# Performance work log

Measured on AMD Instinct MI355X. Metric: run time of the kernel, lower is better.

## Reference

```python
import jax, jax.numpy as jnp
import numpy as np
from jax import lax

DEPTH = 8
D_MODEL = 768
D_INNER = 2 * D_MODEL      # 1536
D_STATE = 16
DT_RANK = 48               # ceil(768/16)
D_CONV = 4
PATCH = 64
IN_CH = 3
IMG_H, IMG_W = 1280, 960
GRID = ((IMG_H - PATCH) // PATCH + 1, (IMG_W - PATCH) // PATCH + 1)  # (20,15)
NUM_PATCHES = GRID[0] * GRID[1]  # 300
MID = NUM_PATCHES // 2           # middle cls-token position
L = NUM_PATCHES + 1              # 301
EPS = 1e-5


def rmsnorm(x, w):
    return x * lax.rsqrt(jnp.mean(x * x, axis=-1, keepdims=True) + EPS) * w


def dwconv_causal(u, w, b):
    # u: (B,L,C), w: (C,k) depthwise, b: (C,) -- causal conv along L
    C = u.shape[-1]
    k = w.shape[-1]
    up = jnp.pad(u, ((0, 0), (k - 1, 0), (0, 0)))
    out = lax.conv_general_dilated(
        up.transpose(0, 2, 1), w[:, None, :], (1,), 'VALID',
        dimension_numbers=('NCH', 'OIH', 'NCH'), feature_group_count=C)
    return out.transpose(0, 2, 1) + b


def ssm_branch(u, convw, convb, Wx, Wdt, bdt, Alog, Dskip):
    # u: (B,L,d_inner) -> selective state-space scan output (B,L,d_inner)
    uc = jax.nn.silu(dwconv_causal(u, convw, convb))
    x_dbl = jnp.einsum('bld,ed->ble', uc, Wx)              # (B,L,dr+2*ds)
    dt, Bm, Cm = jnp.split(x_dbl, [DT_RANK, DT_RANK + D_STATE], axis=-1)
    delta = jax.nn.softplus(jnp.einsum('blr,dr->bld', dt, Wdt) + bdt)  # (B,L,di)
    A = -jnp.exp(Alog)                                     # (di, ds)

    def step(h, inp):
        d_t, B_t, C_t, u_t = inp                           # (B,di),(B,ds),(B,ds),(B,di)
        dA = jnp.exp(d_t[:, :, None] * A)                  # (B,di,ds)
        dBu = d_t[:, :, None] * B_t[:, None, :] * u_t[:, :, None]
        h = dA * h + dBu
        y = jnp.einsum('bds,bs->bd', h, C_t)
        return h, y

    Bsz = u.shape[0]
    h0 = jnp.zeros((Bsz, D_INNER, D_STATE), dtype=u.dtype)
    seq = (delta.transpose(1, 0, 2), Bm.transpose(1, 0, 2),
           Cm.transpose(1, 0, 2), uc.transpose(1, 0, 2))
    _, ys = lax.scan(step, h0, seq)
    return ys.transpose(1, 0, 2) + uc * Dskip


def _forward(x, patch_w, patch_b, cls_token, pos_embed, norm_ws,
             Win, convw_f, convb_f, Wx_f, Wdt_f, bdt_f, Alog_f, Dskip_f,
             convw_b, convb_b, Wx_b, Wdt_b, bdt_b, Alog_b, Dskip_b,
             Wout, normf_w):
    B = x.shape[0]
    # patch embed: Conv2d(3->768, k=64, s=64)
    feat = lax.conv_general_dilated(
        x, patch_w, (PATCH, PATCH), 'VALID',
        dimension_numbers=('NCHW', 'OIHW', 'NCHW')) + patch_b[None, :, None, None]
    tok = feat.reshape(B, D_MODEL, NUM_PATCHES).transpose(0, 2, 1)  # (B,300,768)
    cls = jnp.broadcast_to(cls_token, (B, 1, D_MODEL))
    tokens = jnp.concatenate([tok[:, :MID], cls, tok[:, MID:]], axis=1) + pos_embed

    def layer_step(carry, p):
        (nw, W_in, cwf, cbf, Wxf, Wdtf, bdtf, Alf, Df,
         cwb, cbb, Wxb, Wdtb, bdtb, Alb, Db, W_out) = p
        hidden, residual = carry
        residual = residual + hidden
        h = rmsnorm(residual, nw)
        xz = jnp.einsum('bld,ed->ble', h, W_in)            # (B,L,2*di)
        xs, z = jnp.split(xz, 2, axis=-1)
        yf = ssm_branch(xs, cwf, cbf, Wxf, Wdtf, bdtf, Alf, Df)
        yb = ssm_branch(xs[:, ::-1], cwb, cbb, Wxb, Wdtb, bdtb, Alb, Db)[:, ::-1]
        y = (yf + yb) * jax.nn.silu(z)
        out = jnp.einsum('ble,de->bld', y, W_out) / 2.0    # if_divide_out=True
        return (out, residual), None

    params = (norm_ws, Win, convw_f, convb_f, Wx_f, Wdt_f, bdt_f, Alog_f, Dskip_f,
              convw_b, convb_b, Wx_b, Wdt_b, bdt_b, Alog_b, Dskip_b, Wout)
    (hidden, residual), _ = lax.scan(
        layer_step, (tokens, jnp.zeros_like(tokens)), params)
    return rmsnorm(residual + hidden, normf_w)


def setup_inputs() -> dict:
    key = jax.random.key(0)
    ks = jax.random.split(key, 24)
    B = 2
    s = 0.02
    inv_sp = float(np.log(np.expm1(0.01)))  # softplus^-1(0.01)
    inp = {
        'x': jax.random.normal(ks[0], (B, IN_CH, IMG_H, IMG_W), jnp.float32),
        'patch_w': jax.random.normal(ks[1], (D_MODEL, IN_CH, PATCH, PATCH), jnp.float32) * s,
        'patch_b': jnp.zeros((D_MODEL,), jnp.float32),
        'cls_token': jax.random.normal(ks[2], (1, 1, D_MODEL), jnp.float32) * s,
        'pos_embed': jax.random.normal(ks[3], (1, L, D_MODEL), jnp.float32) * s,
        'norm_ws': jnp.ones((DEPTH, D_MODEL), jnp.float32),
        'Win': jax.random.normal(ks[4], (DEPTH, 2 * D_INNER, D_MODEL), jnp.float32) * s,
        'convw_f': jax.random.normal(ks[5], (DEPTH, D_INNER, D_CONV), jnp.float32) * 0.2,
        'convb_f': jnp.zeros((DEPTH, D_INNER), jnp.float32),
        'Wx_f': jax.random.normal(ks[6], (DEPTH, DT_RANK + 2 * D_STATE, D_INNER), jnp.float32) * s,
        'Wdt_f': jax.random.normal(ks[7], (DEPTH, D_INNER, DT_RANK), jnp.float32) * 0.1,
        'bdt_f': jnp.full((DEPTH, D_INNER), inv_sp, jnp.float32),
        'Alog_f': jnp.broadcast_to(jnp.log(jnp.arange(1, D_STATE + 1, dtype=jnp.float32)), (DEPTH, D_INNER, D_STATE)).copy(),
        'Dskip_f': jnp.ones((DEPTH, D_INNER), jnp.float32),
        'convw_b': jax.random.normal(ks[8], (DEPTH, D_INNER, D_CONV), jnp.float32) * 0.2,
        'convb_b': jnp.zeros((DEPTH, D_INNER), jnp.float32),
        'Wx_b': jax.random.normal(ks[9], (DEPTH, DT_RANK + 2 * D_STATE, D_INNER), jnp.float32) * s,
        'Wdt_b': jax.random.normal(ks[10], (DEPTH, D_INNER, DT_RANK), jnp.float32) * 0.1,
        'bdt_b': jnp.full((DEPTH, D_INNER), inv_sp, jnp.float32),
        'Alog_b': jnp.broadcast_to(jnp.log(jnp.arange(1, D_STATE + 1, dtype=jnp.float32)), (DEPTH, D_INNER, D_STATE)).copy(),
        'Dskip_b': jnp.ones((DEPTH, D_INNER), jnp.float32),
        'Wout': jax.random.normal(ks[11], (DEPTH, D_MODEL, D_INNER), jnp.float32) * s,
        'normf_w': jnp.ones((D_MODEL,), jnp.float32),
    }
    return inp


def reference(x, patch_w, patch_b, cls_token, pos_embed, norm_ws,
              Win, convw_f, convb_f, Wx_f, Wdt_f, bdt_f, Alog_f, Dskip_f,
              convw_b, convb_b, Wx_b, Wdt_b, bdt_b, Alog_b, Dskip_b,
              Wout, normf_w):
    return _forward(x, patch_w, patch_b, cls_token, pos_embed, norm_ws,
                    Win, convw_f, convb_f, Wx_f, Wdt_f, bdt_f, Alog_f, Dskip_f,
                    convw_b, convb_b, Wx_b, Wdt_b, bdt_b, Alog_b, Dskip_b,
                    Wout, normf_w)
```

## Files before the change

kernel.cpp:

```cpp
#include <hip/hip_runtime.h>
#include <hip/hip_bf16.h>
#include <math.h>

typedef unsigned short ushort_t;
typedef __attribute__((ext_vector_type(8))) short bf16x8;
typedef __attribute__((ext_vector_type(4))) float f32x4;

#define B_    2
#define L_    301
#define MID_  150
#define DM_   768
#define DI_   1536
#define DS_   16
#define DR_   48
#define XD_   80
#define NP_   300
#define EPS_  1e-5f
#define TP_   40

__device__ __forceinline__ float bf2f(ushort_t u) {
  union { float f; unsigned int i; } v; v.i = ((unsigned int)u) << 16; return v.f;
}
__device__ __forceinline__ ushort_t f2bf(float f) {
  __hip_bfloat16 h = __float2bfloat16(f);
  return *reinterpret_cast<ushort_t*>(&h);
}
__device__ __forceinline__ float silu_f(float x) { return x / (1.f + __expf(-x)); }
__device__ __forceinline__ float softplus_f(float x) {
  return fmaxf(x, 0.f) + log1pf(__expf(-fabsf(x)));
}

__device__ __forceinline__ float ld1(const void* p, size_t i, int bf) {
  if (bf) return bf2f(((const ushort_t*)p)[i]);
  return ((const float*)p)[i];
}
__device__ __forceinline__ float4 ld4(const void* p, size_t i, int bf) {
  if (bf) {
    uint2 r = *(const uint2*)((const ushort_t*)p + i);
    return make_float4(bf2f((ushort_t)(r.x & 0xffffu)), bf2f((ushort_t)(r.x >> 16)),
                       bf2f((ushort_t)(r.y & 0xffffu)), bf2f((ushort_t)(r.y >> 16)));
  }
  return *(const float4*)((const float*)p + i);
}

__device__ __forceinline__ float quad_sum(float x) {
  int a = __builtin_amdgcn_mov_dpp(__float_as_int(x), 0xB1, 0xF, 0xF, true);
  float s = x + __int_as_float(a);
  int b = __builtin_amdgcn_mov_dpp(__float_as_int(s), 0x4E, 0xF, 0xF, true);
  return s + __int_as_float(b);
}

__global__ void detect_dtype(const unsigned int* __restrict__ w, int* __restrict__ flag) {
  *flag = (w[0] == 0x3F803F80u) ? 1 : 0;
}

__global__ __launch_bounds__(256) void gemm64(
    const void* A0, const void* A1, int abf, int lda,
    const void* W0, const void* W1, size_t Woff,
    void* C0, void* C1, int cbf, int ldc,
    const void* bias0, const void* bias1, size_t boff,
    int M, int N, int K, int kc_len, int nbr,
    int mode, float scale,
    const ushort_t* gyf0, const ushort_t* gyb0, const ushort_t* gz,
    const void* nwp, size_t nwoff,
    const int* __restrict__ dflag)
{
  const int bf = *dflag;
  const int br = blockIdx.z % nbr;
  const int kc = blockIdx.z / nbr;
  const void* A = br ? A1 : A0;
  const void* W = br ? W1 : W0;
  void* C = br ? C1 : C0;
  const void* bias = br ? bias1 : bias0;

  __shared__ ushort_t sA[64 * TP_];
  __shared__ ushort_t sW[64 * TP_];

  const int m0 = blockIdx.x * 64, n0 = blockIdx.y * 64;
  const int t = threadIdx.x;
  const int lane = t & 63, wave = t >> 6;
  const int l16 = lane & 15, quad = lane >> 4;
  const int srow = t >> 2, scol = (t & 3) * 8;

  const int gm = m0 + srow;
  size_t grb = 0, grbrev = 0;
  if (gyf0 && gm < M) {
    int gb = gm / L_, gl = gm % L_;
    grb = (size_t)(gb * L_ + gl);
    grbrev = (size_t)(gb * L_ + (L_ - 1 - gl));
  }

  float s_scale = 0.f;
  if (nwp) {
    float ss = 0.f;
    if (gm < M) {
      const float* ar = (const float*)A + (size_t)gm * lda;
      for (int j = (t & 3) * 4; j < K; j += 16) {
        float4 v = *(const float4*)&ar[j];
        ss = fmaf(v.x, v.x, ss); ss = fmaf(v.y, v.y, ss);
        ss = fmaf(v.z, v.z, ss); ss = fmaf(v.w, v.w, ss);
      }
    }
    ss += __shfl_xor(ss, 1);
    ss += __shfl_xor(ss, 2);
    s_scale = rsqrtf(ss / (float)K + EPS_);
  }

  f32x4 acc[4];
#pragma unroll
  for (int i = 0; i < 4; ++i) acc[i] = (f32x4){0.f, 0.f, 0.f, 0.f};

  const int kstart = kc * kc_len;
  const int kend = (kstart + kc_len < K) ? (kstart + kc_len) : K;

  ushort_t tA[8] __attribute__((aligned(16)));
  ushort_t tW[8] __attribute__((aligned(16)));

  auto stageA = [&](int k0) {
    int m = m0 + srow;
    if (m < M) {
      if (gyf0) {
#pragma unroll
        for (int q = 0; q < 8; q += 4) {
          int k = k0 + scol + q;
          if (k + 4 <= kend) {
            float4 vf = ld4(gyf0, grb * DI_ + k, 1);
            float4 vb = ld4(gyb0, grbrev * DI_ + k, 1);
            float4 vz = ld4(gz, grb * (2 * DI_) + DI_ + k, 1);
            tA[q+0] = f2bf((vf.x + vb.x) * silu_f(vz.x));
            tA[q+1] = f2bf((vf.y + vb.y) * silu_f(vz.y));
            tA[q+2] = f2bf((vf.z + vb.z) * silu_f(vz.z));
            tA[q+3] = f2bf((vf.w + vb.w) * silu_f(vz.w));
          } else { tA[q+0]=0; tA[q+1]=0; tA[q+2]=0; tA[q+3]=0; }
        }
      } else if (nwp) {
#pragma unroll
        for (int q = 0; q < 8; q += 4) {
          int k = k0 + scol + q;
          if (k + 4 <= kend) {
            float4 v = *(const float4*)((const float*)A + (size_t)m * lda + k);
            tA[q+0] = f2bf(v.x * s_scale * ld1(nwp, nwoff + k + 0, bf));
            tA[q+1] = f2bf(v.y * s_scale * ld1(nwp, nwoff + k + 1, bf));
            tA[q+2] = f2bf(v.z * s_scale * ld1(nwp, nwoff + k + 2, bf));
            tA[q+3] = f2bf(v.w * s_scale * ld1(nwp, nwoff + k + 3, bf));
          } else { tA[q+0]=0; tA[q+1]=0; tA[q+2]=0; tA[q+3]=0; }
        }
      } else {
#pragma unroll
        for (int q = 0; q < 8; q += 4) {
          int k = k0 + scol + q;
          float4 v = (k + 4 <= kend) ? ld4(A, (size_t)m * lda + k, abf)
                                     : make_float4(0.f, 0.f, 0.f, 0.f);
          tA[q+0]=f2bf(v.x); tA[q+1]=f2bf(v.y); tA[q+2]=f2bf(v.z); tA[q+3]=f2bf(v.w);
        }
      }
    } else {
#pragma unroll
      for (int q = 0; q < 8; ++q) tA[q] = 0;
    }
  };
  auto stageW = [&](int k0) {
    int n = n0 + srow;
    if (n < N) {
#pragma unroll
      for (int q = 0; q < 8; q += 4) {
        int k = k0 + scol + q;
        float4 v = (k + 4 <= kend) ? ld4(W, Woff + (size_t)n * K + k, bf)
                                   : make_float4(0.f, 0.f, 0.f, 0.f);
        tW[q+0]=f2bf(v.x); tW[q+1]=f2bf(v.y); tW[q+2]=f2bf(v.z); tW[q+3]=f2bf(v.w);
      }
    } else {
#pragma unroll
      for (int q = 0; q < 8; ++q) tW[q] = 0;
    }
  };

  stageA(kstart); stageW(kstart);
  for (int k0 = kstart; k0 < kend; k0 += 32) {
    *(uint4*)&sA[srow * TP_ + scol] = *(const uint4*)tA;
    *(uint4*)&sW[srow * TP_ + scol] = *(const uint4*)tW;
    __syncthreads();
    int kn = k0 + 32;
    if (kn >= kend) kn = kstart;
    stageA(kn); stageW(kn);
    bf16x8 bw = *(const bf16x8*)&sW[(wave * 16 + l16) * TP_ + quad * 8];
#pragma unroll
    for (int i = 0; i < 4; ++i) {
      bf16x8 af = *(const bf16x8*)&sA[(i * 16 + l16) * TP_ + quad * 8];
      acc[i] = __builtin_amdgcn_mfma_f32_16x16x32_bf16(af, bw, acc[i], 0, 0, 0);
    }
    __syncthreads();
  }

  int n = n0 + wave * 16 + l16;
  if (n < N) {
    float bval = (mode == 1) ? ld1(bias, boff + n, bf) : 0.f;
#pragma unroll
    for (int i = 0; i < 4; ++i) {
#pragma unroll
      for (int r = 0; r < 4; ++r) {
        int m = m0 + i * 16 + quad * 4 + r;
        if (m >= M) continue;
        float v = acc[i][r] * scale;
        if (mode == 1) v = softplus_f(v + bval);
        if (mode == 2) atomicAdd((float*)C + (size_t)m * ldc + n, v);
        else if (cbf)  ((ushort_t*)C)[(size_t)m * ldc + n] = f2bf(v);
        else           ((float*)C)[(size_t)m * ldc + n] = v;
      }
    }
  }
}

__global__ __launch_bounds__(256) void gemm_patch_mfma(
    const void* __restrict__ X, const void* __restrict__ Wp,
    float* __restrict__ rawp, const int* __restrict__ dflag)
{
  const int bf = *dflag;
  __shared__ ushort_t sA[64 * TP_];
  __shared__ ushort_t sW[128 * TP_];

  const int m0 = blockIdx.x * 64, n0 = blockIdx.y * 128;
  const int kbase = blockIdx.z * 1024;
  const int t = threadIdx.x;
  const int lane = t & 63, wave = t >> 6;
  const int l16 = lane & 15, quad = lane >> 4;

  const int srowA = t >> 2, scolA = (t & 3) * 8;
  const int srowW = t >> 1, scolW = (t & 1) * 16;

  const int m = m0 + srowA;
  const int bb = m / NP_, p = m % NP_;
  const int ph = p / 15, pw = p % 15;
  const bool mok = (m < 600);

  f32x4 acc[4][2];
#pragma unroll
  for (int i = 0; i < 4; ++i)
#pragma unroll
    for (int j = 0; j < 2; ++j) acc[i][j] = (f32x4){0.f, 0.f, 0.f, 0.f};

  ushort_t tA[8] __attribute__((aligned(16)));
  ushort_t tW[16] __attribute__((aligned(16)));

  auto stageA = [&](int kc) {
    if (mok) {
      int k = kbase + kc + scolA;
      int c = k >> 12, ky = (k >> 6) & 63, kx = k & 63;
      size_t xi = ((size_t)((bb * 3 + c) * 1280 + ph * 64 + ky)) * 960 + pw * 64 + kx;
#pragma unroll
      for (int q = 0; q < 8; q += 4) {
        float4 v = ld4(X, xi + q, bf);
        tA[q+0]=f2bf(v.x); tA[q+1]=f2bf(v.y); tA[q+2]=f2bf(v.z); tA[q+3]=f2bf(v.w);
      }
    } else {
#pragma unroll
      for (int q = 0; q < 8; ++q) tA[q] = 0;
    }
  };
  auto stageW = [&](int kc) {
    int n = n0 + srowW;
    size_t wb = (size_t)n * 12288 + kbase + kc + scolW;
#pragma unroll
    for (int q = 0; q < 16; q += 4) {
      float4 v = ld4(Wp, wb + q, bf);
      tW[q+0]=f2bf(v.x); tW[q+1]=f2bf(v.y); tW[q+2]=f2bf(v.z); tW[q+3]=f2bf(v.w);
    }
  };

  stageA(0); stageW(0);
  for (int kc = 0; kc < 1024; kc += 32) {
    *(uint4*)&sA[srowA * TP_ + scolA] = *(const uint4*)tA;
    *(uint4*)&sW[srowW * TP_ + scolW]     = *(const uint4*)&tW[0];
    *(uint4*)&sW[srowW * TP_ + scolW + 8] = *(const uint4*)&tW[8];
    __syncthreads();
    int kn = (kc + 32 < 1024) ? kc + 32 : 0;
    stageA(kn); stageW(kn);

    bf16x8 af[4], bw[2];
#pragma unroll
    for (int i = 0; i < 4; ++i)
      af[i] = *(const bf16x8*)&sA[(i * 16 + l16) * TP_ + quad * 8];
#pragma unroll
    for (int j = 0; j < 2; ++j)
      bw[j] = *(const bf16x8*)&sW[(wave * 32 + j * 16 + l16) * TP_ + quad * 8];
#pragma unroll
    for (int i = 0; i < 4; ++i)
#pragma unroll
      for (int j = 0; j < 2; ++j)
        acc[i][j] = __builtin_amdgcn_mfma_f32_16x16x32_bf16(af[i], bw[j], acc[i][j], 0, 0, 0);
    __syncthreads();
  }

#pragma unroll
  for (int i = 0; i < 4; ++i) {
#pragma unroll
    for (int r = 0; r < 4; ++r) {
      int mm = m0 + i * 16 + quad * 4 + r;
      if (mm >= 600) continue;
#pragma unroll
      for (int j = 0; j < 2; ++j) {
        int nn = n0 + wave * 32 + j * 16 + l16;
        atomicAdd(&rawp[(size_t)mm * DM_ + nn], acc[i][j][r]);
      }
    }
  }
}

__global__ void assemble_tokens(const float* __restrict__ rawp,
                                const void* __restrict__ patch_b,
                                const void* __restrict__ cls,
                                const void* __restrict__ pos,
                                float* __restrict__ residual,
                                const int* __restrict__ dflag)
{
  const int bf = *dflag;
  int idx = blockIdx.x * 256 + threadIdx.x;
  int d = idx % DM_;
  int bl = idx / DM_;
  int l = bl % L_;
  int b = bl / L_;
  float v;
  if (l == MID_) v = ld1(cls, d, bf);
  else {
    int pp = (l < MID_) ? l : l - 1;
    v = ld1(patch_b, d, bf) + rawp[(size_t)(b * NP_ + pp) * DM_ + d];
  }
  v += ld1(pos, (size_t)l * DM_ + d, bf);
  residual[idx] = v;
}

__global__ void conv_silu(const ushort_t* __restrict__ xz,
                          const void* __restrict__ cwf, const void* __restrict__ cbf,
                          const void* __restrict__ cwb, const void* __restrict__ cbb,
                          size_t cwoff, size_t cboff,
                          ushort_t* __restrict__ ucf, ushort_t* __restrict__ ucb,
                          float* __restrict__ xdz,
                          const int* __restrict__ dflag)
{
  const int bf = *dflag;
  int idx = blockIdx.x * 256 + threadIdx.x;
  if (idx < 96320) xdz[idx] = 0.f;
  int d = idx % DI_;
  int bl = idx / DI_;
  int l = bl % L_;
  int b = bl / L_;
  float af = ld1(cbf, cboff + d, bf);
#pragma unroll
  for (int k = 0; k < 4; ++k) {
    int lo = l - 3 + k;
    if (lo >= 0) af += ld1(cwf, cwoff + d * 4 + k, bf) * bf2f(xz[((size_t)(b * L_ + lo)) * (2*DI_) + d]);
  }
  ucf[idx] = f2bf(silu_f(af));
  float ab = ld1(cbb, cboff + d, bf);
#pragma unroll
  for (int k = 0; k < 4; ++k) {
    int j = l - 3 + k;
    if (j >= 0) ab += ld1(cwb, cwoff + d * 4 + k, bf) * bf2f(xz[((size_t)(b * L_ + (L_ - 1 - j))) * (2*DI_) + d]);
  }
  ucb[idx] = f2bf(silu_f(ab));
}

__global__ __launch_bounds__(256) void scan_kernel(
    const ushort_t* __restrict__ uc0, ushort_t* __restrict__ dl0, const float* __restrict__ xd0,
    const ushort_t* __restrict__ uc1, ushort_t* __restrict__ dl1, const float* __restrict__ xd1,
    const void* __restrict__ Al_f, const void* __restrict__ Dk_f,
    const void* __restrict__ Al_b, const void* __restrict__ Dk_b,
    const void* __restrict__ Wdt_f, const void* __restrict__ Wdt_b,
    const void* __restrict__ bdt_f, const void* __restrict__ bdt_b,
    size_t Aoff, size_t Doff, size_t Wdtoff, size_t bdtoff,
    const int* __restrict__ dflag)
{
  const int bf = *dflag;
  const int b = blockIdx.y;
  const int br = blockIdx.z;
  const ushort_t* uc = br ? uc1 : uc0;
  ushort_t* dl = br ? dl1 : dl0;
  const float* xd = br ? xd1 : xd0;
  const void* Al = br ? Al_b : Al_f;
  const void* Dk = br ? Dk_b : Dk_f;
  const void* Wd = br ? Wdt_b : Wdt_f;
  const void* bd = br ? bdt_b : bdt_f;

  __shared__ ushort_t     sXD[304 * 72];
  __shared__ unsigned int sDU[302 * 64];
  __shared__ float        sBC[302 * 32];

  const int t = threadIdx.x;
  for (int i = t; i < 304 * 8; i += 256) {
    int l = i >> 3, q = i & 7;
    ushort_t tmp[8] __attribute__((aligned(16)));
#pragma unroll
    for (int j = 0; j < 8; ++j) {
      int c = q * 8 + j;
      float v = (l < L_ && c < DR_) ? xd[(size_t)(b * L_ + l) * XD_ + c] : 0.f;
      tmp[j] = f2bf(v);
    }
    *(uint4*)&sXD[l * 72 + q * 8] = *(const uint4*)tmp;
  }
  for (int i = t; i < 302 * 8; i += 256) {
    int l = i >> 3, q = i & 7;
    float4 v = (l < L_) ? *(const float4*)&xd[(size_t)(b * L_ + l) * XD_ + DR_ + q * 4]
                        : make_float4(0.f, 0.f, 0.f, 0.f);
    *(float4*)&sBC[l * 32 + q * 4] = v;
  }
  __syncthreads();

  {
    const int lane = t & 63, wave = t >> 6;
    const int l16 = lane & 15, quad = lane >> 4;
    const int chx = wave * 16 + l16;
    const int dch = blockIdx.x * 64 + chx;
    bf16x8 bwf[2];
#pragma unroll
    for (int kk = 0; kk < 2; ++kk) {
      ushort_t tmp[8] __attribute__((aligned(16)));
#pragma unroll
      for (int j = 0; j < 8; ++j) {
        int r = kk * 32 + quad * 8 + j;
        tmp[j] = (r < DR_) ? f2bf(ld1(Wd, Wdtoff + (size_t)dch * DR_ + r, bf)) : (ushort_t)0;
      }
      bwf[kk] = *(const bf16x8*)tmp;
    }
    const float bv = ld1(bd, bdtoff + dch, bf);
    for (int mt = 0; mt < 19; ++mt) {
      f32x4 acc = (f32x4){0.f, 0.f, 0.f, 0.f};
#pragma unroll
      for (int kk = 0; kk < 2; ++kk) {
        bf16x8 af = *(const bf16x8*)&sXD[(mt * 16 + l16) * 72 + kk * 32 + quad * 8];
        acc = __builtin_amdgcn_mfma_f32_16x16x32_bf16(af, bwf[kk], acc, 0, 0, 0);
      }
#pragma unroll
      for (int rr = 0; rr < 4; ++rr) {
        int row = mt * 16 + quad * 4 + rr;
        if (row < 302)
          *(ushort_t*)((char*)&sDU[row * 64 + chx] + 2) = f2bf(softplus_f(acc[rr] + bv));
      }
    }
  }
  {
    const int d0 = blockIdx.x * 64;
    for (int i = t; i < 302 * 8; i += 256) {
      int l = i >> 3, q = i & 7;
      ushort_t uw[8] __attribute__((aligned(16))) = {0,0,0,0,0,0,0,0};
      if (l < L_) *(uint4*)uw = *(const uint4*)&uc[(size_t)(b * L_ + l) * DI_ + d0 + q * 8];
#pragma unroll
      for (int j = 0; j < 8; ++j)
        *(ushort_t*)((char*)&sDU[l * 64 + q * 8 + j] + 0) = uw[j];
    }
  }
  __syncthreads();

  const int ch = t >> 2;
  const int sl = t & 3;
  const int d = blockIdx.x * 64 + ch;
  float Areg[4], h[4];
#pragma unroll
  for (int s = 0; s < 4; ++s) {
    Areg[s] = -__expf(ld1(Al, Aoff + (size_t)d * 16 + sl * 4 + s, bf));
    h[s] = 0.f;
  }
  const float Dsk = ld1(Dk, Doff + d, bf);

  size_t idx = (size_t)(b * L_) * DI_ + d;
  unsigned int w0 = sDU[ch];
  float dt = __int_as_float(w0 & 0xFFFF0000u);
  float u  = __int_as_float(w0 << 16);
  float4 bB = *(const float4*)&sBC[sl * 4];
  float4 bC = *(const float4*)&sBC[16 + sl * 4];
  for (int l = 0; l < L_; ++l) {
    unsigned int wn = sDU[(l + 1) * 64 + ch];
    float4 nB = *(const float4*)&sBC[(l + 1) * 32 + sl * 4];
    float4 nC = *(const float4*)&sBC[(l + 1) * 32 + 16 + sl * 4];
    float du = dt * u;
    float dA0 = __expf(dt * Areg[0]);
    float dA1 = __expf(dt * Areg[1]);
    float dA2 = __expf(dt * Areg[2]);
    float dA3 = __expf(dt * Areg[3]);
    h[0] = fmaf(dA0, h[0], du * bB.x);
    h[1] = fmaf(dA1, h[1], du * bB.y);
    h[2] = fmaf(dA2, h[2], du * bB.z);
    h[3] = fmaf(dA3, h[3], du * bB.w);
    float yv = fmaf(h[0], bC.x, fmaf(h[1], bC.y, fmaf(h[2], bC.z, h[3] * bC.w)));
    yv = quad_sum(yv);
    dl[idx] = f2bf(yv + u * Dsk);
    dt = __int_as_float(wn & 0xFFFF0000u);
    u  = __int_as_float(wn << 16);
    bB = nB; bC = nC;
    idx += DI_;
  }
}

__global__ __launch_bounds__(256) void final_norm(
    const float* __restrict__ residual,
    const void* __restrict__ nfw, void* __restrict__ out,
    const int* __restrict__ dflag)
{
  const int bf = *dflag;
  const int row = blockIdx.x;
  const int t = threadIdx.x;
  const size_t base = (size_t)row * DM_;
  float v[3];
  float ss = 0.f;
#pragma unroll
  for (int i = 0; i < 3; ++i) {
    int c = t + i * 256;
    float x = residual[base + c];
    v[i] = x;
    ss += x * x;
  }
#pragma unroll
  for (int off = 32; off > 0; off >>= 1) ss += __shfl_down(ss, off);
  __shared__ float ps[4];
  if ((t & 63) == 0) ps[t >> 6] = ss;
  __syncthreads();
  float rs = rsqrtf((ps[0] + ps[1] + ps[2] + ps[3]) / (float)DM_ + EPS_);
#pragma unroll
  for (int i = 0; i < 3; ++i) {
    int c = t + i * 256;
    float val = v[i] * rs * ld1(nfw, c, bf);
    if (bf) ((__hip_bfloat16*)out)[base + c] = __float2bfloat16(val);
    else    ((float*)out)[base + c] = val;
  }
}

extern "C" void kernel_launch(void* const* d_in, const int* in_sizes, int n_in,
                              void* d_out, int out_size, void* d_ws, size_t ws_size,
                              hipStream_t stream)
{
  const void* X        = d_in[0];
  const void* patch_w  = d_in[1];
  const void* patch_b  = d_in[2];
  const void* cls      = d_in[3];
  const void* pos      = d_in[4];
  const void* norm_ws  = d_in[5];
  const void* Win      = d_in[6];
  const void* convw_f  = d_in[7];
  const void* convb_f  = d_in[8];
  const void* Wx_f     = d_in[9];
  const void* Wdt_f    = d_in[10];
  const void* bdt_f    = d_in[11];
  const void* Alog_f   = d_in[12];
  const void* Dskip_f  = d_in[13];
  const void* convw_b  = d_in[14];
  const void* convb_b  = d_in[15];
  const void* Wx_b     = d_in[16];
  const void* Wdt_b    = d_in[17];
  const void* bdt_b    = d_in[18];
  const void* Alog_b   = d_in[19];
  const void* Dskip_b  = d_in[20];
  const void* Wout     = d_in[21];
  const void* normf_w  = d_in[22];

  const int BL = B_ * L_;

  char* base = (char*)d_ws;
  int*      dflag    = (int*)(base + 0);
  float*    residual = (float*)(base + 1849600);
  ushort_t* xz       = (ushort_t*)(base + 4623616);
  ushort_t* ucf      = (ushort_t*)(base + 8322304);
  ushort_t* ucb      = (ushort_t*)(base + 10171648);
  ushort_t* dlf      = (ushort_t*)(base + 12020992);
  ushort_t* dlb      = (ushort_t*)(base + 13870336);
  float*    xdf      = (float*)(base + 15719680);
  float*    xdb      = (float*)(base + 15912320);
  float*    rawp     = (float*)(base + 4623616);
  ushort_t* yf       = dlf;
  ushort_t* yb       = dlb;

  detect_dtype<<<1, 1, 0, stream>>>((const unsigned int*)norm_ws, dflag);

  hipMemsetAsync(rawp, 0, 600 * DM_ * 4, stream);
  gemm_patch_mfma<<<dim3(10, 6, 12), 256, 0, stream>>>(X, patch_w, rawp, dflag);
  assemble_tokens<<<(BL * DM_) / 256, 256, 0, stream>>>(rawp, patch_b, cls, pos, residual, dflag);

  for (int layer = 0; layer < 8; ++layer) {
    size_t nwoff   = (size_t)layer * DM_;
    size_t Winoff  = (size_t)layer * 2 * DI_ * DM_;
    size_t cwoff   = (size_t)layer * DI_ * 4;
    size_t cboff   = (size_t)layer * DI_;
    size_t Wxoff   = (size_t)layer * XD_ * DI_;
    size_t Wdtoff  = (size_t)layer * DI_ * DR_;
    size_t bdtoff  = (size_t)layer * DI_;
    size_t Aloff   = (size_t)layer * DI_ * DS_;
    size_t Dkoff   = (size_t)layer * DI_;
    size_t Woutoff = (size_t)layer * DM_ * DI_;

    gemm64<<<dim3(10, 48, 1), 256, 0, stream>>>(
        residual, residual, 0, DM_, Win, Win, Winoff, xz, xz, 1, 2 * DI_,
        nullptr, nullptr, 0, BL, 2 * DI_, DM_, DM_, 1, 0, 1.f,
        nullptr, nullptr, nullptr, norm_ws, nwoff, dflag);

    conv_silu<<<(BL * DI_) / 256, 256, 0, stream>>>(xz, convw_f, convb_f, convw_b, convb_b,
                                                    cwoff, cboff, ucf, ucb, xdf, dflag);

    gemm64<<<dim3(10, 2, 16), 256, 0, stream>>>(
        ucf, ucb, 1, DI_, Wx_f, Wx_b, Wxoff, xdf, xdb, 0, XD_,
        nullptr, nullptr, 0, BL, XD_, DI_, 192, 2, 2, 1.f,
        nullptr, nullptr, nullptr, nullptr, 0, dflag);

    scan_kernel<<<dim3(24, 2, 2), 256, 0, stream>>>(ucf, dlf, xdf, ucb, dlb, xdb,
                                                    Alog_f, Dskip_f, Alog_b, Dskip_b,
                                                    Wdt_f, Wdt_b, bdt_f, bdt_b,
                                                    Aloff, Dkoff, Wdtoff, bdtoff, dflag);

    gemm64<<<dim3(10, 12, 4), 256, 0, stream>>>(
        dlf, dlf, 1, DI_, Wout, Wout, Woutoff, residual, residual, 0, DM_,
        nullptr, nullptr, 0, BL, DM_, DI_, 384, 1, 2, 0.5f,
        yf, yb, xz, nullptr, 0, dflag);
  }

  final_norm<<<BL, 256, 0, stream>>>(residual, normf_w, d_out, dflag);
}
```

Before: 1.701 ms.

## Split scan state across 16 lanes per channel and stage outputs in LDS

The selective-scan kernel now gives each channel 16 lanes, one state element per lane, instead of 4 lanes holding 4 states each. Blocks cover 32 channels with 512 threads, which doubles the grid and quadruples the total thread count. This shortens the per-thread serial work in each step and exposes more waves to hide latency on the sequential length-301 recurrence. In exchange, the cross-lane reduction grows from 2 to 4 DPP steps per step. Per-step results are written to shared memory by a single lane and then stored to global memory in a coalesced pass after the scan, replacing the strided per-step global stores.

```diff
diff --git a/kernel.cpp b/kernel.cpp
--- a/kernel.cpp
+++ b/kernel.cpp
@@ -43,11 +43,15 @@
   return *(const float4*)((const float*)p + i);
 }
 
-__device__ __forceinline__ float quad_sum(float x) {
-  int a = __builtin_amdgcn_mov_dpp(__float_as_int(x), 0xB1, 0xF, 0xF, true);
+__device__ __forceinline__ float row16_sum(float x) {
+  int a = __builtin_amdgcn_mov_dpp(__float_as_int(x), 0x128, 0xF, 0xF, true);
   float s = x + __int_as_float(a);
-  int b = __builtin_amdgcn_mov_dpp(__float_as_int(s), 0x4E, 0xF, 0xF, true);
-  return s + __int_as_float(b);
+  int b = __builtin_amdgcn_mov_dpp(__float_as_int(s), 0x124, 0xF, 0xF, true);
+  s = s + __int_as_float(b);
+  int c = __builtin_amdgcn_mov_dpp(__float_as_int(s), 0xB1, 0xF, 0xF, true);
+  s = s + __int_as_float(c);
+  int d = __builtin_amdgcn_mov_dpp(__float_as_int(s), 0x4E, 0xF, 0xF, true);
+  return s + __int_as_float(d);
 }
 
 __global__ void detect_dtype(const unsigned int* __restrict__ w, int* __restrict__ flag) {
@@ -360,7 +364,7 @@
   ucb[idx] = f2bf(silu_f(ab));
 }
 
-__global__ __launch_bounds__(256) void scan_kernel(
+__global__ __launch_bounds__(512) void scan_kernel(
     const ushort_t* __restrict__ uc0, ushort_t* __restrict__ dl0, const float* __restrict__ xd0,
     const ushort_t* __restrict__ uc1, ushort_t* __restrict__ dl1, const float* __restrict__ xd1,
     const void* __restrict__ Al_f, const void* __restrict__ Dk_f,
@@ -382,11 +386,12 @@
   const void* bd = br ? bdt_b : bdt_f;
 
   __shared__ ushort_t     sXD[304 * 72];
-  __shared__ unsigned int sDU[302 * 64];
+  __shared__ unsigned int sDU[302 * 32];
   __shared__ float        sBC[302 * 32];
+  ushort_t* sY = sXD;
 
   const int t = threadIdx.x;
-  for (int i = t; i < 304 * 8; i += 256) {
+  for (int i = t; i < 304 * 8; i += 512) {
     int l = i >> 3, q = i & 7;
     ushort_t tmp[8] __attribute__((aligned(16)));
 #pragma unroll
@@ -397,7 +402,7 @@
     }
     *(uint4*)&sXD[l * 72 + q * 8] = *(const uint4*)tmp;
   }
-  for (int i = t; i < 302 * 8; i += 256) {
+  for (int i = t; i < 302 * 8; i += 512) {
     int l = i >> 3, q = i & 7;
     float4 v = (l < L_) ? *(const float4*)&xd[(size_t)(b * L_ + l) * XD_ + DR_ + q * 4]
                         : make_float4(0.f, 0.f, 0.f, 0.f);
@@ -408,21 +413,22 @@
   {
     const int lane = t & 63, wave = t >> 6;
     const int l16 = lane & 15, quad = lane >> 4;
-    const int chx = wave * 16 + l16;
-    const int dch = blockIdx.x * 64 + chx;
-    bf16x8 bwf[2];
-#pragma unroll
-    for (int kk = 0; kk < 2; ++kk) {
-      ushort_t tmp[8] __attribute__((aligned(16)));
-#pragma unroll
-      for (int j = 0; j < 8; ++j) {
-        int r = kk * 32 + quad * 8 + j;
-        tmp[j] = (r < DR_) ? f2bf(ld1(Wd, Wdtoff + (size_t)dch * DR_ + r, bf)) : (ushort_t)0;
-      }
-      bwf[kk] = *(const bf16x8*)tmp;
-    }
-    const float bv = ld1(bd, bdtoff + dch, bf);
-    for (int mt = 0; mt < 19; ++mt) {
+    for (int job = wave; job < 38; job += 8) {
+      int mt = job >> 1, nt = job & 1;
+      int chx = nt * 16 + l16;
+      int dch = blockIdx.x * 32 + chx;
+      bf16x8 bwf[2];
+#pragma unroll
+      for (int kk = 0; kk < 2; ++kk) {
+        ushort_t tmp[8] __attribute__((aligned(16)));
+#pragma unroll
+        for (int j = 0; j < 8; ++j) {
+          int r = kk * 32 + quad * 8 + j;
+          tmp[j] = (r < DR_) ? f2bf(ld1(Wd, Wdtoff + (size_t)dch * DR_ + r, bf)) : (ushort_t)0;
+        }
+        bwf[kk] = *(const bf16x8*)tmp;
+      }
+      const float bv = ld1(bd, bdtoff + dch, bf);
       f32x4 acc = (f32x4){0.f, 0.f, 0.f, 0.f};
 #pragma unroll
       for (int kk = 0; kk < 2; ++kk) {
@@ -433,60 +439,55 @@
       for (int rr = 0; rr < 4; ++rr) {
         int row = mt * 16 + quad * 4 + rr;
         if (row < 302)
-          *(ushort_t*)((char*)&sDU[row * 64 + chx] + 2) = f2bf(softplus_f(acc[rr] + bv));
+          *(ushort_t*)((char*)&sDU[row * 32 + chx] + 2) = f2bf(softplus_f(acc[rr] + bv));
       }
     }
   }
   {
-    const int d0 = blockIdx.x * 64;
-    for (int i = t; i < 302 * 8; i += 256) {
-      int l = i >> 3, q = i & 7;
+    const int d0 = blockIdx.x * 32;
+    for (int i = t; i < 302 * 4; i += 512) {
+      int l = i >> 2, q = i & 3;
       ushort_t uw[8] __attribute__((aligned(16))) = {0,0,0,0,0,0,0,0};
       if (l < L_) *(uint4*)uw = *(const uint4*)&uc[(size_t)(b * L_ + l) * DI_ + d0 + q * 8];
 #pragma unroll
       for (int j = 0; j < 8; ++j)
-        *(ushort_t*)((char*)&sDU[l * 64 + q * 8 + j] + 0) = uw[j];
+        *(ushort_t*)((char*)&sDU[l * 32 + q * 8 + j] + 0) = uw[j];
     }
   }
   __syncthreads();
 
-  const int ch = t >> 2;
-  const int sl = t & 3;
-  const int d = blockIdx.x * 64 + ch;
-  float Areg[4], h[4];
-#pragma unroll
-  for (int s = 0; s < 4; ++s) {
-    Areg[s] = -__expf(ld1(Al, Aoff + (size_t)d * 16 + sl * 4 + s, bf));
-    h[s] = 0.f;
-  }
+  const int ch = t >> 4;
+  const int sl = t & 15;
+  const int d = blockIdx.x * 32 + ch;
+  float Areg = -__expf(ld1(Al, Aoff + (size_t)d * 16 + sl, bf));
+  float h = 0.f;
   const float Dsk = ld1(Dk, Doff + d, bf);
 
-  size_t idx = (size_t)(b * L_) * DI_ + d;
   unsigned int w0 = sDU[ch];
   float dt = __int_as_float(w0 & 0xFFFF0000u);
   float u  = __int_as_float(w0 << 16);
-  float4 bB = *(const float4*)&sBC[sl * 4];
-  float4 bC = *(const float4*)&sBC[16 + sl * 4];
+  float bB = sBC[sl];
+  float bC = sBC[16 + sl];
   for (int l = 0; l < L_; ++l) {
-    unsigned int wn = sDU[(l + 1) * 64 + ch];
-    float4 nB = *(const float4*)&sBC[(l + 1) * 32 + sl * 4];
-    float4 nC = *(const float4*)&sBC[(l + 1) * 32 + 16 + sl * 4];
-    float du = dt * u;
-    float dA0 = __expf(dt * Areg[0]);
-    float dA1 = __expf(dt * Areg[1]);
-    float dA2 = __expf(dt * Areg[2]);
-    float dA3 = __expf(dt * Areg[3]);
-    h[0] = fmaf(dA0, h[0], du * bB.x);
-    h[1] = fmaf(dA1, h[1], du * bB.y);
-    h[2] = fmaf(dA2, h[2], du * bB.z);
-    h[3] = fmaf(dA3, h[3], du * bB.w);
-    float yv = fmaf(h[0], bC.x, fmaf(h[1], bC.y, fmaf(h[2], bC.z, h[3] * bC.w)));
-    yv = quad_sum(yv);
-    dl[idx] = f2bf(yv + u * Dsk);
+    unsigned int wn = sDU[(l + 1) * 32 + ch];
+    float nB = sBC[(l + 1) * 32 + sl];
+    float nC = sBC[(l + 1) * 32 + 16 + sl];
+    float dA = __expf(dt * Areg);
+    h = fmaf(dA, h, (dt * u) * bB);
+    float yv = row16_sum(h * bC);
+    if (sl == 0) sY[l * 32 + ch] = f2bf(yv + u * Dsk);
     dt = __int_as_float(wn & 0xFFFF0000u);
     u  = __int_as_float(wn << 16);
     bB = nB; bC = nC;
-    idx += DI_;
+  }
+  __syncthreads();
+
+  {
+    const int d0 = blockIdx.x * 32;
+    for (int i = t; i < L_ * 32; i += 512) {
+      int l = i >> 5, c = i & 31;
+      dl[(size_t)(b * L_ + l) * DI_ + d0 + c] = sY[l * 32 + c];
+    }
   }
 }
 
@@ -598,7 +599,7 @@
         nullptr, nullptr, 0, BL, XD_, DI_, 192, 2, 2, 1.f,
         nullptr, nullptr, nullptr, nullptr, 0, dflag);
 
-    scan_kernel<<<dim3(24, 2, 2), 256, 0, stream>>>(ucf, dlf, xdf, ucb, dlb, xdb,
+    scan_kernel<<<dim3(48, 2, 2), 512, 0, stream>>>(ucf, dlf, xdf, ucb, dlb, xdb,
                                                     Alog_f, Dskip_f, Alog_b, Dskip_b,
                                                     Wdt_f, Wdt_b, bdt_f, bdt_b,
                                                     Aloff, Dkoff, Wdtoff, bdtoff, dflag);
```

Result: faster. 1.636 ms (-3.8%).
